# Kernel tuning notes

Measured on AMD Instinct MI355X. Metric: run time of the kernel, lower is better.

## Reference

```python
import jax, jax.numpy as jnp
import numpy as np

B, H, W = 128, 48, 48
CEN_IN, CEN_OUT, DIR_IN, DIR_OUT, CEN_K, DIR_K = 32, 32, 24, 24, 3, 5
C_IN = CEN_IN + 4 * DIR_IN  # central + 4 directional groups (hor, ver, diag, anti-diag)


def _dwconv(x, k):
    # x: [B, C, H, W], k: [C, kh, kw] depthwise kernels -> SAME-padded depthwise conv
    C = x.shape[1]
    return jax.lax.conv_general_dilated(
        x, k[:, None], window_strides=(1, 1), padding='SAME',
        dimension_numbers=('NCHW', 'OIHW', 'NCHW'), feature_group_count=C)


def setup_inputs() -> dict:
    key = jax.random.key(0)
    ks = jax.random.split(key, 8)
    s = 0.1
    return {
        'x': jax.random.normal(ks[0], (B, C_IN, H, W), dtype=jnp.float32),
        'cen_tensor': jax.random.normal(ks[1], (CEN_IN, CEN_K, CEN_K), dtype=jnp.float32) * s,
        'dir_tensor': jax.random.normal(ks[2], (DIR_IN, DIR_K), dtype=jnp.float32) * s,
        'cen2cen': jax.random.normal(ks[3], (CEN_OUT, CEN_IN), dtype=jnp.float32) * s,
        'par2cen': jax.random.normal(ks[4], (CEN_OUT, DIR_IN), dtype=jnp.float32) * s,
        'dia2cen': jax.random.normal(ks[5], (CEN_OUT, DIR_IN), dtype=jnp.float32) * s,
        'cen2dir': jax.random.normal(ks[6], (DIR_OUT, CEN_IN), dtype=jnp.float32) * s,
        'dir2dir': jax.random.normal(ks[7], (DIR_OUT, DIR_IN), dtype=jnp.float32) * s,
    }


def reference(x, cen_tensor, dir_tensor, cen2cen, par2cen, dia2cen, cen2dir, dir2dir):
    cen_in = cen_tensor.shape[0]
    dir_in, K = dir_tensor.shape
    # split channel groups: [cen | hor | ver | diag | anti-diag]
    xc = x[:, :cen_in]
    xh = x[:, cen_in:cen_in + dir_in]
    xv = x[:, cen_in + dir_in:cen_in + 2 * dir_in]
    xd1 = x[:, cen_in + 2 * dir_in:cen_in + 3 * dir_in]
    xd2 = x[:, cen_in + 3 * dir_in:]
    eye = jnp.eye(K, dtype=x.dtype)
    # --- directional depthwise stage ---
    yc = _dwconv(xc, cen_tensor)                                # full 2D kernel per channel
    yh = _dwconv(xh, dir_tensor[:, None, :])
    yv = _dwconv(xv, dir_tensor[:, :, None])                    # K x 1 vertical line
    yd1 = _dwconv(xd1, dir_tensor[:, :, None] * eye)            # main diagonal line
    yd2 = _dwconv(xd2, dir_tensor[:, :, None] * eye[:, ::-1])   # anti-diagonal line
    # --- directional pointwise (1x1) mixing stage ---
    mix = lambda Wm, t: jnp.einsum('oc,bchw->bohw', Wm, t)
    out_cen = mix(cen2cen, yc) + mix(par2cen, yh + yv) + mix(dia2cen, yd1 + yd2)
    od_cen = mix(cen2dir, yc)
    out_dirs = [od_cen + mix(dir2dir, t) for t in (yh, yv, yd1, yd2)]
    return jnp.concatenate([out_cen] + out_dirs, axis=1)
```

## Files before the change

### kernel.cpp

```cpp
#include <hip/hip_runtime.h>
#include <hip/hip_bf16.h>


namespace {
constexpr int HH = 48, WW = 48, HW = HH * WW;
constexpr int C_IN = 128, C_OUT = 128, NB = 128;
constexpr int RPB = 8;
constexpr int NSTR = HH / RPB;
constexpr int PIX = RPB * WW;
constexpr int NT = 512;
constexpr int CHK = 16;
constexpr int NCHK = C_IN / CHK;
constexpr int XR = RPB + 4;
constexpr int QR = 17;
constexpr int XROWF = QR * 4;
constexpr int XQ = CHK * XR * QR;
constexpr int YCS = 392;
constexpr int NBLK = NB * NSTR;
constexpr size_t M_BYTES = 128 * 128 * 2;
constexpr size_t ZB_OFF = M_BYTES;
}

typedef __attribute__((ext_vector_type(8))) short bf16x8;
typedef __attribute__((ext_vector_type(4))) float f32x4;

__device__ __forceinline__ ushort f2bf(float f) {
    __hip_bfloat16 h = __float2bfloat16(f);
    return *reinterpret_cast<ushort*>(&h);
}

__global__ void build_M(const float* __restrict__ c2c, const float* __restrict__ p2c,
                        const float* __restrict__ d2c, const float* __restrict__ c2d,
                        const float* __restrict__ d2dW, ushort* __restrict__ Mbf) {
    int t = blockIdx.x * 256 + threadIdx.x;
    if (t >= 128 * 128) return;
    int o = t & 127, c = t >> 7;
    float v;
    if (o < 32) {
        if (c < 32)       v = c2c[o * 32 + c];
        else if (c < 56)  v = p2c[o * 24 + c - 32];
        else if (c < 80)  v = p2c[o * 24 + c - 56];
        else if (c < 104) v = d2c[o * 24 + c - 80];
        else              v = d2c[o * 24 + c - 104];
    } else {
        int g = (o - 32) / 24, oo = (o - 32) % 24;
        if (c < 32) v = c2d[oo * 32 + c];
        else {
            int gc = (c - 32) / 24, cc2 = (c - 32) % 24;
            v = (gc == g) ? d2dW[oo * 24 + cc2] : 0.f;
        }
    }
    Mbf[o * 128 + c] = f2bf(v);
}

__global__ __launch_bounds__(NT) void dsc_fused(
    const float* __restrict__ x,
    const float* __restrict__ cen_t,
    const float* __restrict__ dir_t,
    const ushort* __restrict__ Mbf,
    const float* __restrict__ zb,
    float* __restrict__ out)
{
    __shared__ float  xs[XQ * 4];
    __shared__ ushort yT[PIX * 128];
    __shared__ ushort ycp[CHK * YCS];

    const int tid = threadIdx.x;
    const int bid = (blockIdx.x & 7) * (NBLK / 8) + (blockIdx.x >> 3);
    const int b   = bid / NSTR;
    const int h0  = (bid % NSTR) * RPB;
    const float* __restrict__ xb = x + (size_t)b * C_IN * HW;

    auto stage = [&](int t) {
        const int c0 = t * CHK;
#pragma unroll
        for (int k = 0; k < 7; ++k) {
            int d = tid + k * NT;
            if (d < XQ) {
                int q  = d % QR;
                int cr = d / QR;
                int r  = cr % XR;
                int c  = cr / XR;
                int gh = h0 - 2 + r;
                bool ok = ((unsigned)gh < (unsigned)HH) && (q < 12);
                const float* src = ok ? (xb + (size_t)(c0 + c) * HW + gh * WW + q * 4) : zb;
                __builtin_amdgcn_global_load_lds(
                    (const __attribute__((address_space(1))) unsigned int*)src,
                    (__attribute__((address_space(3))) unsigned int*)(xs + (size_t)d * 4),
                    16, 0, 0);
            }
        }
    };

    auto dwconv = [&](int t) {
        const int c0 = t * CHK;
#pragma unroll
        for (int k = 0; k < 2; ++k) {
            int task = tid + k * NT;
            if (task >= CHK * 48) break;
            int c   = task / 48;
            int pg  = task % 48;
            int row = pg & 7;
            int w0  = (pg >> 3) * 8;
            int cc  = c0 + c;
            const float* xr0 = xs + (size_t)(c * XR) * XROWF;
            float acc[8];
#pragma unroll
            for (int j = 0; j < 8; ++j) acc[j] = 0.f;

            if (cc < 32) {
#pragma unroll
                for (int i = 0; i < 3; ++i) {
                    const float* xr = xr0 + (row + 1 + i) * XROWF;
                    float4 A = *(const float4*)&xr[(w0 - 4) & 63];
                    float4 B = *(const float4*)&xr[w0];
                    float4 C = *(const float4*)&xr[w0 + 4];
                    float4 D = *(const float4*)&xr[(w0 + 8) & 63];
                    float win[16] = {A.x,A.y,A.z,A.w, B.x,B.y,B.z,B.w,
                                     C.x,C.y,C.z,C.w, D.x,D.y,D.z,D.w};
                    float k0 = cen_t[cc*9 + i*3 + 0];
                    float k1 = cen_t[cc*9 + i*3 + 1];
                    float k2 = cen_t[cc*9 + i*3 + 2];
#pragma unroll
                    for (int j = 0; j < 8; ++j)
                        acc[j] += k0*win[j+3] + k1*win[j+4] + k2*win[j+5];
                }
            } else if (cc < 56) {
                int cd = cc - 32;
                const float* xr = xr0 + (row + 2) * XROWF;
                float4 A = *(const float4*)&xr[(w0 - 4) & 63];
                float4 B = *(const float4*)&xr[w0];
                float4 C = *(const float4*)&xr[w0 + 4];
                float4 D = *(const float4*)&xr[(w0 + 8) & 63];
                float win[16] = {A.x,A.y,A.z,A.w, B.x,B.y,B.z,B.w,
                                 C.x,C.y,C.z,C.w, D.x,D.y,D.z,D.w};
#pragma unroll
                for (int i = 0; i < 5; ++i) {
                    float tt = dir_t[cd*5 + i];
#pragma unroll
                    for (int j = 0; j < 8; ++j) acc[j] += tt * win[j+2+i];
                }
            } else if (cc < 80) {
                int cd = cc - 56;
#pragma unroll
                for (int i = 0; i < 5; ++i) {
                    const float* xr = xr0 + (row + i) * XROWF;
                    float4 B = *(const float4*)&xr[w0];
                    float4 C = *(const float4*)&xr[w0 + 4];
                    float w8[8] = {B.x,B.y,B.z,B.w, C.x,C.y,C.z,C.w};
                    float tt = dir_t[cd*5 + i];
#pragma unroll
                    for (int j = 0; j < 8; ++j) acc[j] += tt * w8[j];
                }
            } else {
                int cd  = (cc < 104) ? cc - 80 : cc - 104;
                bool d1 = (cc < 104);
#pragma unroll
                for (int i = 0; i < 5; ++i) {
                    const float* xr = xr0 + (row + i) * XROWF;
                    float4 A = *(const float4*)&xr[(w0 - 4) & 63];
                    float4 B = *(const float4*)&xr[w0];
                    float4 C = *(const float4*)&xr[w0 + 4];
                    float4 D = *(const float4*)&xr[(w0 + 8) & 63];
                    float win[16] = {A.x,A.y,A.z,A.w, B.x,B.y,B.z,B.w,
                                     C.x,C.y,C.z,C.w, D.x,D.y,D.z,D.w};
                    float tt = dir_t[cd*5 + i];
                    if (d1) {
#pragma unroll
                        for (int j = 0; j < 8; ++j) acc[j] += tt * win[j+2+i];
                    } else {
#pragma unroll
                        for (int j = 0; j < 8; ++j) acc[j] += tt * win[j+6-i];
                    }
                }
            }

            union { ushort us[8]; uint4 v4; } s;
#pragma unroll
            for (int j = 0; j < 8; ++j) s.us[j] = f2bf(acc[j]);
            *(uint4*)&ycp[c * YCS + row * 48 + w0] = s.v4;
        }
    };

    auto transpose = [&](int t) {
#pragma unroll
        for (int k = 0; k < 2; ++k) {
            int task = tid + k * NT;
            if (task >= 2 * PIX) break;
            int gg = task / PIX;
            int p  = task % PIX;
            int g  = t * 2 + gg;
            union { ushort us[8]; uint4 v4; } s;
#pragma unroll
            for (int j = 0; j < 8; ++j) s.us[j] = ycp[(gg * 8 + j) * YCS + p];
            int byte = p * 256 + ((g ^ (p & 7)) << 4);
            *(uint4*)((char*)yT + byte) = s.v4;
        }
    };

    stage(0);
    __syncthreads();
    for (int t = 0; t < NCHK; ++t) {
        dwconv(t);
        __syncthreads();
        if (t + 1 < NCHK) stage(t + 1);
        transpose(t);
        __syncthreads();
    }

    const int l     = tid & 63;
    const int wv    = tid >> 6;
    const int ofr   = wv & 3;
    const int phalf = wv >> 2;
    float* __restrict__ ob = out + (size_t)b * C_OUT * HW + h0 * WW;

#pragma unroll
    for (int pass = 0; pass < 2; ++pass) {
        int o0 = pass * 64 + ofr * 16;
        bf16x8 afr[4];
#pragma unroll
        for (int kb = 0; kb < 4; ++kb)
            afr[kb] = *(const bf16x8*)(Mbf + (o0 + (l & 15)) * 128 + kb * 32 + (l >> 4) * 8);
        f32x4 acc[12] = {};
#pragma unroll
        for (int kb = 0; kb < 4; ++kb) {
            int g = kb * 4 + (l >> 4);
#pragma unroll
            for (int pf = 0; pf < 12; ++pf) {
                int p = (phalf * 12 + pf) * 16 + (l & 15);
                const bf16x8 bfr = *(const bf16x8*)((const char*)yT + p * 256 + ((g ^ (p & 7)) << 4));
                acc[pf] = __builtin_amdgcn_mfma_f32_16x16x32_bf16(afr[kb], bfr, acc[pf], 0, 0, 0);
            }
        }
#pragma unroll
        for (int pf = 0; pf < 12; ++pf) {
            int p = (phalf * 12 + pf) * 16 + (l & 15);
            int obase = o0 + (l >> 4) * 4;
#pragma unroll
            for (int r = 0; r < 4; ++r)
                ob[(size_t)(obase + r) * HW + p] = acc[pf][r];
        }
    }
}

extern "C" void kernel_launch(void* const* d_in, const int* in_sizes, int n_in,
                              void* d_out, int out_size, void* d_ws, size_t ws_size,
                              hipStream_t stream) {
    const float* x     = (const float*)d_in[0];
    const float* cen_t = (const float*)d_in[1];
    const float* dir_t = (const float*)d_in[2];
    const float* c2c   = (const float*)d_in[3];
    const float* p2c   = (const float*)d_in[4];
    const float* d2c   = (const float*)d_in[5];
    const float* c2d   = (const float*)d_in[6];
    const float* d2dW  = (const float*)d_in[7];
    float* out = (float*)d_out;

    ushort* Mbf = (ushort*)d_ws;
    float*  zb  = (float*)((char*)d_ws + ZB_OFF);

    hipMemsetAsync(zb, 0, 64, stream);
    build_M<<<64, 256, 0, stream>>>(c2c, p2c, d2c, c2d, d2dW, Mbf);
    dsc_fused<<<NBLK, NT, 0, stream>>>(x, cen_t, dir_t, Mbf, zb, out);
}
```

Measured before the change: 97.71 us.

## Interleave MFMA pointwise mixing into the channel-chunk loop with split barriers

Moves the bf16 MFMA pointwise mixing into the channel-chunk loop, running one K-block after every two chunks once its transposed activations are ready. Both output passes now accumulate at the same time (2x12 accumulators), so each B fragment from LDS is read once and the tail after the loop only stores. The single __syncthreads is replaced by separate LDS-wait and global-load-wait barriers with scheduling fences, so MFMA work can overlap the async staging of the next chunk. In exchange, register pressure rises from 48 to 96 accumulator floats, which may hurt occupancy or cause spills at 512 threads, and the A fragments are reloaded from global memory inside the loop.

```diff
diff --git a/kernel.cpp b/kernel.cpp
--- a/kernel.cpp
+++ b/kernel.cpp
@@ -28,6 +28,8 @@
     __hip_bfloat16 h = __float2bfloat16(f);
     return *reinterpret_cast<ushort*>(&h);
 }
+
+#define SFENCE() __builtin_amdgcn_sched_barrier(0)
 
 __global__ void build_M(const float* __restrict__ c2c, const float* __restrict__ p2c,
                         const float* __restrict__ d2c, const float* __restrict__ c2d,
@@ -71,6 +73,11 @@
     const int h0  = (bid % NSTR) * RPB;
     const float* __restrict__ xb = x + (size_t)b * C_IN * HW;
 
+    const int l     = tid & 63;
+    const int wv    = tid >> 6;
+    const int ofr   = wv & 3;
+    const int phalf = wv >> 2;
+
     auto stage = [&](int t) {
         const int c0 = t * CHK;
 #pragma unroll
@@ -104,9 +111,9 @@
             int w0  = (pg >> 3) * 8;
             int cc  = c0 + c;
             const float* xr0 = xs + (size_t)(c * XR) * XROWF;
-            float acc[8];
-#pragma unroll
-            for (int j = 0; j < 8; ++j) acc[j] = 0.f;
+            float acv[8];
+#pragma unroll
+            for (int j = 0; j < 8; ++j) acv[j] = 0.f;
 
             if (cc < 32) {
 #pragma unroll
@@ -123,7 +130,7 @@
                     float k2 = cen_t[cc*9 + i*3 + 2];
 #pragma unroll
                     for (int j = 0; j < 8; ++j)
-                        acc[j] += k0*win[j+3] + k1*win[j+4] + k2*win[j+5];
+                        acv[j] += k0*win[j+3] + k1*win[j+4] + k2*win[j+5];
                 }
             } else if (cc < 56) {
                 int cd = cc - 32;
@@ -138,7 +145,7 @@
                 for (int i = 0; i < 5; ++i) {
                     float tt = dir_t[cd*5 + i];
 #pragma unroll
-                    for (int j = 0; j < 8; ++j) acc[j] += tt * win[j+2+i];
+                    for (int j = 0; j < 8; ++j) acv[j] += tt * win[j+2+i];
                 }
             } else if (cc < 80) {
                 int cd = cc - 56;
@@ -150,7 +157,7 @@
                     float w8[8] = {B.x,B.y,B.z,B.w, C.x,C.y,C.z,C.w};
                     float tt = dir_t[cd*5 + i];
 #pragma unroll
-                    for (int j = 0; j < 8; ++j) acc[j] += tt * w8[j];
+                    for (int j = 0; j < 8; ++j) acv[j] += tt * w8[j];
                 }
             } else {
                 int cd  = (cc < 104) ? cc - 80 : cc - 104;
@@ -167,17 +174,17 @@
                     float tt = dir_t[cd*5 + i];
                     if (d1) {
 #pragma unroll
-                        for (int j = 0; j < 8; ++j) acc[j] += tt * win[j+2+i];
+                        for (int j = 0; j < 8; ++j) acv[j] += tt * win[j+2+i];
                     } else {
 #pragma unroll
-                        for (int j = 0; j < 8; ++j) acc[j] += tt * win[j+6-i];
+                        for (int j = 0; j < 8; ++j) acv[j] += tt * win[j+6-i];
                     }
                 }
             }
 
             union { ushort us[8]; uint4 v4; } s;
 #pragma unroll
-            for (int j = 0; j < 8; ++j) s.us[j] = f2bf(acc[j]);
+            for (int j = 0; j < 8; ++j) s.us[j] = f2bf(acv[j]);
             *(uint4*)&ycp[c * YCS + row * 48 + w0] = s.v4;
         }
     };
@@ -198,6 +205,23 @@
         }
     };
 
+    f32x4 acc[2][12] = {};
+
+    auto mfma_kb = [&](int kb) {
+        int g = kb * 4 + (l >> 4);
+#pragma unroll
+        for (int pf = 0; pf < 12; ++pf) {
+            int p = (phalf * 12 + pf) * 16 + (l & 15);
+            const bf16x8 bfr = *(const bf16x8*)((const char*)yT + p * 256 + ((g ^ (p & 7)) << 4));
+#pragma unroll
+            for (int pass = 0; pass < 2; ++pass) {
+                int o0 = pass * 64 + ofr * 16;
+                bf16x8 a = *(const bf16x8*)(Mbf + (o0 + (l & 15)) * 128 + kb * 32 + (l >> 4) * 8);
+                acc[pass][pf] = __builtin_amdgcn_mfma_f32_16x16x32_bf16(a, bfr, acc[pass][pf], 0, 0, 0);
+            }
+        }
+    };
+
     stage(0);
     __syncthreads();
     for (int t = 0; t < NCHK; ++t) {
@@ -205,40 +229,28 @@
         __syncthreads();
         if (t + 1 < NCHK) stage(t + 1);
         transpose(t);
-        __syncthreads();
+        asm volatile("s_waitcnt lgkmcnt(0)" ::: "memory");
+        SFENCE();
+        __builtin_amdgcn_s_barrier();
+        SFENCE();
+        if (t & 1) mfma_kb(t >> 1);
+        asm volatile("s_waitcnt vmcnt(0)" ::: "memory");
+        SFENCE();
+        __builtin_amdgcn_s_barrier();
+        SFENCE();
     }
 
-    const int l     = tid & 63;
-    const int wv    = tid >> 6;
-    const int ofr   = wv & 3;
-    const int phalf = wv >> 2;
     float* __restrict__ ob = out + (size_t)b * C_OUT * HW + h0 * WW;
-
 #pragma unroll
     for (int pass = 0; pass < 2; ++pass) {
         int o0 = pass * 64 + ofr * 16;
-        bf16x8 afr[4];
-#pragma unroll
-        for (int kb = 0; kb < 4; ++kb)
-            afr[kb] = *(const bf16x8*)(Mbf + (o0 + (l & 15)) * 128 + kb * 32 + (l >> 4) * 8);
-        f32x4 acc[12] = {};
-#pragma unroll
-        for (int kb = 0; kb < 4; ++kb) {
-            int g = kb * 4 + (l >> 4);
-#pragma unroll
-            for (int pf = 0; pf < 12; ++pf) {
-                int p = (phalf * 12 + pf) * 16 + (l & 15);
-                const bf16x8 bfr = *(const bf16x8*)((const char*)yT + p * 256 + ((g ^ (p & 7)) << 4));
-                acc[pf] = __builtin_amdgcn_mfma_f32_16x16x32_bf16(afr[kb], bfr, acc[pf], 0, 0, 0);
-            }
-        }
 #pragma unroll
         for (int pf = 0; pf < 12; ++pf) {
             int p = (phalf * 12 + pf) * 16 + (l & 15);
             int obase = o0 + (l >> 4) * 4;
 #pragma unroll
             for (int r = 0; r < 4; ++r)
-                ob[(size_t)(obase + r) * HW + p] = acc[pf][r];
+                ob[(size_t)(obase + r) * HW + p] = acc[pass][pf][r];
         }
     }
 }
```

Result: slower. 109.9 us (+12.5%).
